# Kernel tuning notes

Hardware: AMD Instinct MI355X
Metric: run time of the kernel (lower is better)

## Reference

```python
import jax, jax.numpy as jnp
import numpy as np

B = 64        # num_groups
G = 32        # group_size
D = 2000      # output dim (counts per bin/gene)
M = 16        # m_samples
E = 16        # noise_dim
DIN = 256
LAM = 1.0
TRUST = 0.25
SMOOTH = 1e-8
IPF_ITERS = 60
EPS = 1e-12


def _arch(x, noise, W, b):
    # simple linear architecture: concat(x, noise) @ W + b
    return jnp.concatenate([x, noise], axis=-1) @ W + b


def _loss(x, target, W, b, noise_loss):
    # replicate each row m times (unsqueeze(1).expand(...).reshape == repeat)
    x_rep = jnp.repeat(x, M, axis=0)                      # [n*M, DIN]
    pred = _arch(x_rep, noise_loss, W, b)                 # [n*M, D] (no act_fn in loss path)
    pred = pred.reshape(B, G, M, D).sum(axis=1)           # [B, M, D]
    term_conf = jnp.linalg.norm(pred - target[:, None, :], axis=2).mean(axis=1)  # [B]
    sq = jnp.sum(pred * pred, axis=2)                     # [B, M]
    inn = jnp.einsum('bmd,bnd->bmn', pred, pred)          # [B, M, M]
    sqd = jnp.clip(sq[:, :, None] + sq[:, None, :] - 2.0 * inn, 1e-6)
    d = jnp.sqrt(sqd)
    mask = 1.0 - jnp.eye(M, dtype=d.dtype)
    mean_pd = jnp.sum(d * mask, axis=(1, 2)) / (M * (M - 1))
    return jnp.mean(term_conf - (LAM / 2.0) * mean_pd)


def _ipf(x_pred, C):
    # KL/I-projection with row anchoring (keep_rows=True, trust_clip=0.25)
    y = jnp.clip(x_pred, 0.0)
    C = jnp.clip(C.astype(y.dtype), 0.0)
    R = y.sum(axis=2)                                     # [B, G] anchor row totals
    col_zero = (y.sum(axis=1) <= 0) & (C > 0)
    y = y + SMOOTH * col_zero[:, None, :].astype(y.dtype)
    row_zero = (y.sum(axis=2) <= 0) & (R > 0)
    y = y + SMOOTH * row_zero[:, :, None].astype(y.dtype)

    def body(_, y):
        col = jnp.clip(y.sum(axis=1), EPS)
        y = y * jnp.clip(C / col, 1.0 - TRUST, 1.0 + TRUST)[:, None, :]
        row = jnp.clip(y.sum(axis=2), EPS)
        y = y * jnp.clip(R / row, 1.0 - TRUST, 1.0 + TRUST)[:, :, None]
        return y

    y = jax.lax.fori_loop(0, IPF_ITERS, body, y)
    col = jnp.clip(y.sum(axis=1), EPS)
    return y * (C / col)[:, None, :]


def _rank(v, descending):
    # rank along last axis via double argsort (0 = first picked)
    order = jnp.argsort(-v if descending else v, axis=-1)
    return jnp.argsort(order, axis=-1)


def _round_to_targets(x, target_bd):
    # exact integerization across G per (B, D); jit-safe full-G rank replaces dynamic-k topk+scatter
    x = jnp.clip(x, 0.0)
    xf = jnp.floor(x)
    y = xf.astype(jnp.int32)                              # [B, G, D]
    frac = x - xf
    need = target_bd - y.sum(axis=1)                      # [B, D]
    pos = jnp.clip(need, 0)
    q = pos // G
    y = y + q[:, None, :]
    r = pos - q * G
    rank = _rank(jnp.transpose(frac, (0, 2, 1)), descending=True)   # [B, D, G]
    add = (rank < r[:, :, None]).astype(jnp.int32)
    y = y + jnp.transpose(add, (0, 2, 1))
    # negative residuals: remove from smallest frac among y > 0
    need = target_bd - y.sum(axis=1)
    neg = jnp.clip(-need, 0)
    neg = jnp.minimum(neg, y.sum(axis=1))
    q = neg // G
    y_before = y
    y = jnp.clip(y - q[:, None, :], 0)
    removed = (y_before - y).sum(axis=1)
    r = neg - removed
    frac_m = jnp.where(y > 0, frac, jnp.inf)
    rank = _rank(jnp.transpose(frac_m, (0, 2, 1)), descending=False)
    rem = (rank < r[:, :, None]).astype(jnp.int32)
    y = jnp.clip(y - jnp.transpose(rem, (0, 2, 1)), 0)
    return y


def setup_inputs() -> dict:
    key = jax.random.key(0)
    ks = jax.random.split(key, 6)
    x = jax.random.normal(ks[0], (B * G, DIN), dtype=jnp.float32)
    target = jax.random.uniform(ks[1], (B, D), dtype=jnp.float32) * 100.0
    target_sum = jax.random.randint(ks[2], (B, D), 0, 200, dtype=jnp.int32)
    W = jax.random.normal(ks[3], (DIN + E, D), dtype=jnp.float32) * 0.02
    b = jnp.zeros((D,), dtype=jnp.float32)
    noise_loss = jax.random.normal(ks[4], (B * G * M, E), dtype=jnp.float32)
    noise_sample = jax.random.normal(ks[5], (B * G, E), dtype=jnp.float32)
    return {"x": x, "target": target, "target_sum": target_sum, "W": W, "b": b,
            "noise_loss": noise_loss, "noise_sample": noise_sample}


def reference(x, target, target_sum, W, b, noise_loss, noise_sample):
    loss = _loss(x, target, W, b, noise_loss)
    # conditional_sample pipeline (no-grad in original): softplus act (min_value==0)
    x_pred = jax.nn.softplus(_arch(x, noise_sample, W, b)).reshape(B, G, D)
    y_float = _ipf(x_pred, target_sum.astype(jnp.float32))
    y_int = _round_to_targets(y_float, target_sum.astype(jnp.int32))
    return loss, y_int.reshape(B * G, D)
```

## Files before the change

### kernel.cpp

```cpp
#include <hip/hip_runtime.h>
#include <math.h>

#define NB   64
#define NG   32
#define ND   2000
#define NM   16
#define NE   16
#define NDIN 256
#define NK   272

#define XPT_COLS 1152
#define SP_TAU   424
#define SP_F4_PER_B 6784
#define SMEM_MEGA (4096 + XPT_COLS * 128)

__device__ __forceinline__ float clampf(float v, float lo, float hi) {
    return fminf(fmaxf(v, lo), hi);
}

__device__ __forceinline__ float softplusf(float v) {
    return (v > 20.f) ? v : log1pf(expf(v));
}

__device__ __forceinline__ float readlane_f(float v, int lane) {
    return __int_as_float(__builtin_amdgcn_readlane(__float_as_int(v), lane));
}

__device__ __forceinline__ int sp_idx(int tau, int j, int k) {
    return (j * 8 + k) * SP_TAU + tau;
}

__device__ __forceinline__ int yget(const int* yvp, int g) {
    return (yvp[g >> 2] >> (8 * (g & 3))) & 0xff;
}
__device__ __forceinline__ void yadd(int* yvp, int g, int delta) {
    yvp[g >> 2] += delta << (8 * (g & 3));
}

__device__ __forceinline__ float wave_sum32(float v[NG], int lane) {
    {   const bool hi = (lane & 32) != 0;
        #pragma unroll
        for (int k = 0; k < 16; ++k) {
            float s = hi ? v[k] : v[k + 16];
            float r = __shfl_xor(s, 32);
            v[k] = (hi ? v[k + 16] : v[k]) + r;
        }
    }
    {   const bool hi = (lane & 16) != 0;
        #pragma unroll
        for (int k = 0; k < 8; ++k) {
            float s = hi ? v[k] : v[k + 8];
            float r = __shfl_xor(s, 16);
            v[k] = (hi ? v[k + 8] : v[k]) + r;
        }
    }
    {   const bool hi = (lane & 8) != 0;
        #pragma unroll
        for (int k = 0; k < 4; ++k) {
            float s = hi ? v[k] : v[k + 4];
            float r = __shfl_xor(s, 8);
            v[k] = (hi ? v[k + 4] : v[k]) + r;
        }
    }
    {   const bool hi = (lane & 4) != 0;
        #pragma unroll
        for (int k = 0; k < 2; ++k) {
            float s = hi ? v[k] : v[k + 2];
            float r = __shfl_xor(s, 4);
            v[k] = (hi ? v[k + 2] : v[k]) + r;
        }
    }
    {   const bool hi = (lane & 2) != 0;
        float s = hi ? v[0] : v[1];
        float r = __shfl_xor(s, 2);
        v[0] = (hi ? v[1] : v[0]) + r;
    }
    v[0] += __shfl_xor(v[0], 1);
    return v[0];
}

__device__ __forceinline__ void ipf_path(
        const float* __restrict__ xpT, const float* __restrict__ spB,
        const int* __restrict__ tsum, float* __restrict__ out,
        char* smem, int b, int t) {
    const int lane = t & 63, w = t >> 6;
    const bool lcls  = (t < 576);
    const bool valid = (t < 1000);
    const int g_own = (lane >> 1) & 31;
    const int rot = t & 7;
    const int tau = t - 576;
    const int c0 = lcls ? (2 * t) : (XPT_COLS + 2 * tau);

    float* wred = (float*)smem;
    char* cb = smem + 4096 + (size_t)c0 * 128;
    const float4* gx = (const float4*)(xpT + ((size_t)b * XPT_COLS + c0) * NG);
    const float4* gs = (const float4*)spB + (size_t)b * SP_F4_PER_B;

    float Cc0 = 0.f, Cc1 = 0.f;
    if (valid) {
        const int2 ci = *(const int2*)(tsum + (size_t)b * ND + c0);
        Cc0 = (float)ci.x; Cc1 = (float)ci.y;
    }
    float Ac0 = 1.f, Ac1 = 1.f;
    float Bown = 1.f, Rown;

    {
        float v[NG];
        if (lcls) {
            #pragma unroll
            for (int k = 0; k < 8; ++k) {
                const float4 a = gx[k], c = gx[8 + k];
                const int ro = 16 * ((k + rot) & 7);
                *(float4*)(cb + ro)       = a;
                *(float4*)(cb + 128 + ro) = c;
                v[4*k+0] = a.x + c.x;
                v[4*k+1] = a.y + c.y;
                v[4*k+2] = a.z + c.z;
                v[4*k+3] = a.w + c.w;
            }
        } else if (valid) {
            #pragma unroll
            for (int k = 0; k < 8; ++k) {
                const float4 a = gs[sp_idx(tau, 0, k)];
                const float4 c = gs[sp_idx(tau, 1, k)];
                v[4*k+0] = a.x + c.x;
                v[4*k+1] = a.y + c.y;
                v[4*k+2] = a.z + c.z;
                v[4*k+3] = a.w + c.w;
            }
        } else {
            #pragma unroll
            for (int g = 0; g < NG; ++g) v[g] = 0.f;
        }
        const float tot = wave_sum32(v, lane);
        if (!(lane & 1)) wred[w * NG + g_own] = tot;
        __syncthreads();
        float s = 0.f;
        #pragma unroll
        for (int w2 = 0; w2 < 16; ++w2) s += wred[w2 * NG + g_own];
        Rown = s;
    }

    for (int q = 1; q <= 60; ++q) {
        float s0 = 0.f, s1 = 0.f;
        if (lcls) {
            #pragma unroll
            for (int k = 0; k < 8; ++k) {
                const int ro = 16 * ((k + rot) & 7);
                const float4 a = *(const float4*)(cb + ro);
                const float4 c = *(const float4*)(cb + 128 + ro);
                float bg;
                bg = readlane_f(Bown, 8*k+0); s0 += a.x*bg; s1 += c.x*bg;
                bg = readlane_f(Bown, 8*k+2); s0 += a.y*bg; s1 += c.y*bg;
                bg = readlane_f(Bown, 8*k+4); s0 += a.z*bg; s1 += c.z*bg;
                bg = readlane_f(Bown, 8*k+6); s0 += a.w*bg; s1 += c.w*bg;
            }
        } else if (valid) {
            #pragma unroll
            for (int k = 0; k < 8; ++k) {
                const float4 a = gs[sp_idx(tau, 0, k)];
                const float4 c = gs[sp_idx(tau, 1, k)];
                float bg;
                bg = readlane_f(Bown, 8*k+0); s0 += a.x*bg; s1 += c.x*bg;
                bg = readlane_f(Bown, 8*k+2); s0 += a.y*bg; s1 += c.y*bg;
                bg = readlane_f(Bown, 8*k+4); s0 += a.z*bg; s1 += c.z*bg;
                bg = readlane_f(Bown, 8*k+6); s0 += a.w*bg; s1 += c.w*bg;
            }
        }
        Ac0 *= clampf(Cc0 / fmaxf(Ac0 * s0, 1e-12f), 0.75f, 1.25f);
        Ac1 *= clampf(Cc1 / fmaxf(Ac1 * s1, 1e-12f), 0.75f, 1.25f);

        asm volatile("" ::: "memory");

        float v[NG];
        if (lcls) {
            #pragma unroll
            for (int k = 0; k < 8; ++k) {
                const int ro = 16 * ((k + rot) & 7);
                const float4 a = *(const float4*)(cb + ro);
                const float4 c = *(const float4*)(cb + 128 + ro);
                v[4*k+0] = a.x * Ac0 + c.x * Ac1;
                v[4*k+1] = a.y * Ac0 + c.y * Ac1;
                v[4*k+2] = a.z * Ac0 + c.z * Ac1;
                v[4*k+3] = a.w * Ac0 + c.w * Ac1;
            }
        } else if (valid) {
            #pragma unroll
            for (int k = 0; k < 8; ++k) {
                const float4 a = gs[sp_idx(tau, 0, k)];
                const float4 c = gs[sp_idx(tau, 1, k)];
                v[4*k+0] = a.x * Ac0 + c.x * Ac1;
                v[4*k+1] = a.y * Ac0 + c.y * Ac1;
                v[4*k+2] = a.z * Ac0 + c.z * Ac1;
                v[4*k+3] = a.w * Ac0 + c.w * Ac1;
            }
        } else {
            #pragma unroll
            for (int g = 0; g < NG; ++g) v[g] = 0.f;
        }
        const float tot = wave_sum32(v, lane);
        const int buf = (q & 1) * (16 * NG);
        if (!(lane & 1)) wred[buf + w * NG + g_own] = tot;
        __syncthreads();
        float s = 0.f;
        #pragma unroll
        for (int w2 = 0; w2 < 16; ++w2) s += wred[buf + w2 * NG + g_own];
        Bown *= clampf(Rown / fmaxf(Bown * s, 1e-12f), 0.75f, 1.25f);
    }

    if (!valid) return;

    #pragma unroll
    for (int jj = 0; jj < 2; ++jj) {
        const int c = c0 + jj;
        const float A = jj ? Ac1 : Ac0;
        const int Ci = (int)(jj ? Cc1 : Cc0);
        const float Cf = (float)Ci;

        float c32[NG];
        if (lcls) {
            const char* basej = cb + jj * 128;
            #pragma unroll
            for (int k = 0; k < 8; ++k) {
                const float4 v4 = *(const float4*)(basej + 16 * ((k + rot) & 7));
                c32[4*k+0] = v4.x; c32[4*k+1] = v4.y;
                c32[4*k+2] = v4.z; c32[4*k+3] = v4.w;
            }
        } else {
            #pragma unroll
            for (int k = 0; k < 8; ++k) {
                const float4 v4 = gs[sp_idx(tau, jj, k)];
                c32[4*k+0] = v4.x; c32[4*k+1] = v4.y;
                c32[4*k+2] = v4.z; c32[4*k+3] = v4.w;
            }
        }

        float s = 0.f;
        #pragma unroll
        for (int g = 0; g < NG; ++g) {
            const float z = c32[g] * A * readlane_f(Bown, 2 * g);
            s += z;
            c32[g] = z;
        }
        const float F = Cf / fmaxf(s, 1e-12f);

        int yvp[8];
        #pragma unroll
        for (int i = 0; i < 8; ++i) yvp[i] = 0;
        int isum = 0;
        #pragma unroll
        for (int g = 0; g < NG; ++g) {
            const float y = c32[g] * F;
            const float fl = floorf(y);
            const int yi = (int)fl;
            c32[g] = y - fl;
            yadd(yvp, g, yi);
            isum += yi;
        }
        const int need = Ci - isum;
        const int pos = max(need, 0);
        const int qv = pos >> 5;
        const int rr = pos & 31;
        if (qv > 0) {
            #pragma unroll
            for (int i = 0; i < 8; ++i) yvp[i] += qv * 0x01010101;
        }
        #pragma unroll
        for (int g = 0; g < NG; ++g) {
            const float fg = c32[g];
            int rank = 0;
            #pragma unroll
            for (int h = 0; h < NG; ++h) {
                if (h == g) continue;
                const float fh = c32[h];
                rank += (h < g) ? (fh >= fg ? 1 : 0) : (fh > fg ? 1 : 0);
            }
            if (rank < rr) yadd(yvp, g, 1);
        }
        int neg = max(-need, 0);
        neg = min(neg, isum);
        if (__builtin_expect(neg > 0, 0)) {
            const int q2 = neg >> 5;
            int removed = 0;
            #pragma unroll
            for (int g = 0; g < NG; ++g) {
                const int yb = yget(yvp, g);
                const int yn = max(yb - q2, 0);
                removed += yb - yn;
                yadd(yvp, g, yn - yb);
            }
            const int r2 = neg - removed;
            if (r2 > 0) {
                const float INF = __builtin_inff();
                #pragma unroll
                for (int g = 0; g < NG; ++g) {
                    const float fg = (yget(yvp, g) > 0) ? c32[g] : INF;
                    int rank = 0;
                    #pragma unroll
                    for (int h = 0; h < NG; ++h) {
                        if (h == g) continue;
                        const float fh = (yget(yvp, h) > 0) ? c32[h] : INF;
                        rank += (h < g) ? (fh <= fg ? 1 : 0) : (fh < fg ? 1 : 0);
                    }
                    if (rank < r2) {
                        const int yb = yget(yvp, g);
                        yadd(yvp, g, max(yb - 1, 0) - yb);
                    }
                }
            }
        }
        #pragma unroll
        for (int g = 0; g < NG; ++g)
            out[1 + (size_t)(b * NG + g) * ND + c] = (float)yget(yvp, g);
    }
}

__device__ __forceinline__ void loss_path(
        const float* __restrict__ x, const float* __restrict__ nl,
        const float* __restrict__ tgt, const float* __restrict__ W,
        const float* __restrict__ bias, float* __restrict__ res2,
        float* smem, int cx, int b, int tt) {
    const int half = cx & 1;
    float* xsl = smem;
    float* nsl = smem + 256;
    float* tgl = smem + 512 + half * 4284;
    float* pt  = tgl + 252;

    if (half == 0 && tt < 256) {
        const float* xb = x + (size_t)b * NG * NDIN;
        float s = 0.f;
        for (int g = 0; g < NG; ++g) s += xb[g * NDIN + tt];
        xsl[tt] = s;
        const float* nb = nl + (size_t)b * NG * (NM * NE);
        float s2 = 0.f;
        for (int g = 0; g < NG; ++g) s2 += nb[g * (NM * NE) + tt];
        nsl[tt] = s2;
    }

    int tm = 0, tn = 0;
    if (tt >= 16 && tt < 152) {
        int p = tt - 16;
        for (int m = 0; m < NM; ++m) {
            int c = NM - m;
            if (p < c) { tm = m; tn = m + p; break; }
            p -= c;
        }
    }
    __syncthreads();

    const int d = cx * 250 + tt;
    if (tt < 250) {
        tgl[tt] = tgt[b * ND + d];
        float xw = 0.f;
        #pragma unroll 8
        for (int k = 0; k < NDIN; ++k) xw += xsl[k] * W[(size_t)k * ND + d];
        float we[NE];
        #pragma unroll
        for (int e = 0; e < NE; ++e) we[e] = W[(size_t)(NDIN + e) * ND + d];
        const float base0 = xw + (float)NG * bias[d];
        #pragma unroll
        for (int m = 0; m < NM; ++m) {
            float pm = base0;
            #pragma unroll
            for (int e = 0; e < NE; ++e) pm += nsl[m * NE + e] * we[e];
            pt[m * 252 + tt] = pm;
        }
    }
    if (tt < 32) {
        pt[(tt >> 1) * 252 + 250 + (tt & 1)] = 0.f;
        if (tt < 2) tgl[250 + tt] = 0.f;
    }
    __syncthreads();

    float acc = 0.f;
    if (tt < 16) {
        const float4* pa  = (const float4*)&pt[tt * 252];
        const float4* tga = (const float4*)&tgl[0];
        for (int i = 0; i < 63; ++i) {
            float4 pv = pa[i], tv = tga[i];
            float e0 = pv.x - tv.x, e1 = pv.y - tv.y, e2 = pv.z - tv.z, e3 = pv.w - tv.w;
            acc += e0 * e0 + e1 * e1 + e2 * e2 + e3 * e3;
        }
    } else if (tt < 152) {
        const float4* pa = (const float4*)&pt[tm * 252];
        const float4* pb = (const float4*)&pt[tn * 252];
        for (int i = 0; i < 63; ++i) {
            float4 u = pa[i], v = pb[i];
            acc += u.x * v.x + u.y * v.y + u.z * v.z + u.w * v.w;
        }
    }
    if (tt < 152) res2[((size_t)b * 8 + cx) * 152 + tt] = acc;
}

extern "C" __global__ __launch_bounds__(1024)
void mega(const float* __restrict__ x, const float* __restrict__ nl,
          const float* __restrict__ tgt, const float* __restrict__ W,
          const float* __restrict__ bias, const float* __restrict__ xpT,
          const float* __restrict__ spB, const int* __restrict__ tsum,
          float* __restrict__ out, float* __restrict__ res2) {
    extern __shared__ char smem[];
    const int bid = blockIdx.x;
    const int t = threadIdx.x;
    if (bid < NB) {
        ipf_path(xpT, spB, tsum, out, smem, bid, t);
    } else {
        const int l = bid - NB;
        #pragma unroll
        for (int rep = 0; rep < 2; ++rep) {
            const int slot = l + rep * 192;
            if (slot < 256) {
                __syncthreads();
                const int cx = ((slot & 3) << 1) | (t >> 9);
                loss_path(x, nl, tgt, W, bias, res2, (float*)smem,
                          cx, slot >> 2, t & 511);
            }
        }
    }
}

extern "C" __global__ __launch_bounds__(64)
void k2b_combine(const float* __restrict__ res2, float* __restrict__ out) {
    const int b = blockIdx.x, t = threadIdx.x;
    __shared__ float res[152];
    for (int tau = t; tau < 152; tau += 64) {
        float s = 0.f;
        #pragma unroll
        for (int c = 0; c < 8; ++c) s += res2[((size_t)b * 8 + c) * 152 + tau];
        res[tau] = s;
    }
    __syncthreads();
    if (t == 0) {
        float conf = 0.f;
        for (int m = 0; m < NM; ++m) conf += sqrtf(res[m]);
        conf *= (1.f / NM);
        float pd = 0.f;
        for (int m = 0; m < NM; ++m) {
            const int offm = 16 + m * NM - m * (m - 1) / 2;
            const float sqm = res[offm];
            for (int n = m + 1; n < NM; ++n) {
                const int offn = 16 + n * NM - n * (n - 1) / 2;
                const float sqn = res[offn];
                const float inn = res[offm + (n - m)];
                pd += sqrtf(fmaxf(sqm + sqn - 2.f * inn, 1e-6f));
            }
        }
        pd = 2.f * pd / (float)(NM * (NM - 1));
        atomicAdd(out, (conf - 0.5f * pd) * (1.f / NB));
    }
}

extern "C" __global__ __launch_bounds__(256)
void k3_xpred(const float* __restrict__ x, const float* __restrict__ nsamp,
              const float* __restrict__ W, const float* __restrict__ bias,
              float* __restrict__ xpT, float* __restrict__ spB,
              float* __restrict__ out) {
    const int dx = blockIdx.x;
    const int rb = blockIdx.y;
    const int t  = threadIdx.x;
    if (dx == 0 && rb == 0 && t == 0) out[0] = 0.f;
    __shared__ float xr[8][NK];
    #pragma unroll
    for (int r = 0; r < 8; ++r) {
        const int row = rb * 8 + r;
        xr[r][t] = x[(size_t)row * NDIN + t];
        if (t < NE) xr[r][NDIN + t] = nsamp[row * NE + t];
    }
    __syncthreads();
    if (t >= 250) return;
    const int d = dx * 1000 + 4 * t;
    float acc[8][4];
    #pragma unroll
    for (int r = 0; r < 8; ++r) {
        acc[r][0] = 0.f; acc[r][1] = 0.f; acc[r][2] = 0.f; acc[r][3] = 0.f;
    }
    for (int k = 0; k < NK; k += 4) {
        float4 w[4];
        #pragma unroll
        for (int kk = 0; kk < 4; ++kk) w[kk] = *(const float4*)&W[(size_t)(k + kk) * ND + d];
        #pragma unroll
        for (int r = 0; r < 8; ++r) {
            const float4 xv = *(const float4*)&xr[r][k];
            acc[r][0] += xv.x * w[0].x + xv.y * w[1].x + xv.z * w[2].x + xv.w * w[3].x;
            acc[r][1] += xv.x * w[0].y + xv.y * w[1].y + xv.z * w[2].y + xv.w * w[3].y;
            acc[r][2] += xv.x * w[0].z + xv.y * w[1].z + xv.z * w[2].z + xv.w * w[3].z;
            acc[r][3] += xv.x * w[0].w + xv.y * w[1].w + xv.z * w[2].w + xv.w * w[3].w;
        }
    }
    const float4 bv = *(const float4*)&bias[d];
    const float bvv[4] = {bv.x, bv.y, bv.z, bv.w};
    const int b2 = rb >> 2;
    const int g0 = (rb & 3) * 8;
    #pragma unroll
    for (int dd = 0; dd < 4; ++dd) {
        const int dc = d + dd;
        float4 lo, hi;
        lo.x = softplusf(acc[0][dd] + bvv[dd]);
        lo.y = softplusf(acc[1][dd] + bvv[dd]);
        lo.z = softplusf(acc[2][dd] + bvv[dd]);
        lo.w = softplusf(acc[3][dd] + bvv[dd]);
        hi.x = softplusf(acc[4][dd] + bvv[dd]);
        hi.y = softplusf(acc[5][dd] + bvv[dd]);
        hi.z = softplusf(acc[6][dd] + bvv[dd]);
        hi.w = softplusf(acc[7][dd] + bvv[dd]);
        if (dc < XPT_COLS) {
            float* op = xpT + ((size_t)b2 * XPT_COLS + dc) * NG + g0;
            *(float4*)op       = lo;
            *(float4*)(op + 4) = hi;
        } else {
            float4* sp = (float4*)spB + (size_t)b2 * SP_F4_PER_B;
            const int cc = dc - XPT_COLS;
            const int tau2 = cc >> 1, j = cc & 1;
            const int kk = g0 >> 2;
            sp[sp_idx(tau2, j, kk)]     = lo;
            sp[sp_idx(tau2, j, kk + 1)] = hi;
        }
    }
}

extern "C" void kernel_launch(void* const* d_in, const int* in_sizes, int n_in,
                              void* d_out, int out_size, void* d_ws, size_t ws_size,
                              hipStream_t stream) {
    const float* x     = (const float*)d_in[0];
    const float* tgt   = (const float*)d_in[1];
    const int*   tsum  = (const int*)d_in[2];
    const float* W     = (const float*)d_in[3];
    const float* bias  = (const float*)d_in[4];
    const float* nl    = (const float*)d_in[5];
    const float* nsamp = (const float*)d_in[6];
    float* out = (float*)d_out;

    (void)in_sizes; (void)n_in; (void)out_size; (void)ws_size;

    float* xpT  = (float*)d_ws;
    float* spB  = (float*)((char*)d_ws + 9437184);
    float* res2 = (float*)((char*)d_ws + 16384000);

    static int s_attr_done = 0;
    if (!s_attr_done) {
        hipFuncSetAttribute(reinterpret_cast<const void*>(mega),
                            hipFuncAttributeMaxDynamicSharedMemorySize,
                            SMEM_MEGA);
        s_attr_done = 1;
    }

    hipLaunchKernelGGL(k3_xpred, dim3(2, 256), dim3(256), 0, stream,
                       x, nsamp, W, bias, xpT, spB, out);
    hipLaunchKernelGGL(mega, dim3(256), dim3(1024), SMEM_MEGA, stream,
                       x, nl, tgt, W, bias, xpT, spB, tsum, out, res2);
    hipLaunchKernelGGL(k2b_combine, dim3(NB), dim3(64), 0, stream, res2, out);
}
```

Before: 364.2 us.

## Split IPF rounding epilogue out of mega kernel into separate wide-grid kernel

The per-column rounding epilogue (scale, floor, rank-based remainder distribution) moves out of the 64 IPF blocks of the mega kernel into a new k_epi kernel with an 8x64 grid of 256 threads. The mega kernel now only writes its per-column scale A and per-row scale B into the output buffer as scratch, and k_epi reads them back together with the cached xpT/spB predictions. This spreads the expensive 32x32 rank computation across far more blocks instead of serialising it in the tail of the 64 IPF blocks. The cost is an extra launch, re-reading the predictions from global memory, and relying on the output buffer as a temporary that k_epi later overwrites.

Result: faster. 344.6 us (-5.4%).

```diff
diff --git a/kernel.cpp b/kernel.cpp
--- a/kernel.cpp
+++ b/kernel.cpp
@@ -208,110 +208,14 @@
         Bown *= clampf(Rown / fmaxf(Bown * s, 1e-12f), 0.75f, 1.25f);
     }
 
-    if (!valid) return;
-
-    #pragma unroll
-    for (int jj = 0; jj < 2; ++jj) {
-        const int c = c0 + jj;
-        const float A = jj ? Ac1 : Ac0;
-        const int Ci = (int)(jj ? Cc1 : Cc0);
-        const float Cf = (float)Ci;
-
-        float c32[NG];
-        if (lcls) {
-            const char* basej = cb + jj * 128;
-            #pragma unroll
-            for (int k = 0; k < 8; ++k) {
-                const float4 v4 = *(const float4*)(basej + 16 * ((k + rot) & 7));
-                c32[4*k+0] = v4.x; c32[4*k+1] = v4.y;
-                c32[4*k+2] = v4.z; c32[4*k+3] = v4.w;
-            }
-        } else {
-            #pragma unroll
-            for (int k = 0; k < 8; ++k) {
-                const float4 v4 = gs[sp_idx(tau, jj, k)];
-                c32[4*k+0] = v4.x; c32[4*k+1] = v4.y;
-                c32[4*k+2] = v4.z; c32[4*k+3] = v4.w;
-            }
-        }
-
-        float s = 0.f;
-        #pragma unroll
-        for (int g = 0; g < NG; ++g) {
-            const float z = c32[g] * A * readlane_f(Bown, 2 * g);
-            s += z;
-            c32[g] = z;
-        }
-        const float F = Cf / fmaxf(s, 1e-12f);
-
-        int yvp[8];
-        #pragma unroll
-        for (int i = 0; i < 8; ++i) yvp[i] = 0;
-        int isum = 0;
-        #pragma unroll
-        for (int g = 0; g < NG; ++g) {
-            const float y = c32[g] * F;
-            const float fl = floorf(y);
-            const int yi = (int)fl;
-            c32[g] = y - fl;
-            yadd(yvp, g, yi);
-            isum += yi;
-        }
-        const int need = Ci - isum;
-        const int pos = max(need, 0);
-        const int qv = pos >> 5;
-        const int rr = pos & 31;
-        if (qv > 0) {
-            #pragma unroll
-            for (int i = 0; i < 8; ++i) yvp[i] += qv * 0x01010101;
-        }
-        #pragma unroll
-        for (int g = 0; g < NG; ++g) {
-            const float fg = c32[g];
-            int rank = 0;
-            #pragma unroll
-            for (int h = 0; h < NG; ++h) {
-                if (h == g) continue;
-                const float fh = c32[h];
-                rank += (h < g) ? (fh >= fg ? 1 : 0) : (fh > fg ? 1 : 0);
-            }
-            if (rank < rr) yadd(yvp, g, 1);
-        }
-        int neg = max(-need, 0);
-        neg = min(neg, isum);
-        if (__builtin_expect(neg > 0, 0)) {
-            const int q2 = neg >> 5;
-            int removed = 0;
-            #pragma unroll
-            for (int g = 0; g < NG; ++g) {
-                const int yb = yget(yvp, g);
-                const int yn = max(yb - q2, 0);
-                removed += yb - yn;
-                yadd(yvp, g, yn - yb);
-            }
-            const int r2 = neg - removed;
-            if (r2 > 0) {
-                const float INF = __builtin_inff();
-                #pragma unroll
-                for (int g = 0; g < NG; ++g) {
-                    const float fg = (yget(yvp, g) > 0) ? c32[g] : INF;
-                    int rank = 0;
-                    #pragma unroll
-                    for (int h = 0; h < NG; ++h) {
-                        if (h == g) continue;
-                        const float fh = (yget(yvp, h) > 0) ? c32[h] : INF;
-                        rank += (h < g) ? (fh <= fg ? 1 : 0) : (fh < fg ? 1 : 0);
-                    }
-                    if (rank < r2) {
-                        const int yb = yget(yvp, g);
-                        yadd(yvp, g, max(yb - 1, 0) - yb);
-                    }
-                }
-            }
-        }
-        #pragma unroll
-        for (int g = 0; g < NG; ++g)
-            out[1 + (size_t)(b * NG + g) * ND + c] = (float)yget(yvp, g);
+    if (valid) {
+        float* ap = out + 1 + (size_t)(b * NG) * ND + c0;
+        ap[0] = Ac0; ap[1] = Ac1;
+    }
+    if (w == 0 && !(lane & 1)) {
+        #pragma unroll
+        for (int qq = 0; qq < 8; ++qq)
+            out[1 + (size_t)(b * NG + 1) * ND + qq * 250 + g_own] = Bown;
     }
 }
 
@@ -416,6 +320,124 @@
             }
         }
     }
+}
+
+extern "C" __global__ __launch_bounds__(256)
+void k_epi(const float* __restrict__ xpT, const float* __restrict__ spB,
+           const int* __restrict__ tsum, float* __restrict__ out) {
+    const int chunk = blockIdx.x;
+    const int b     = blockIdx.y;
+    const int tt    = threadIdx.x;
+    __shared__ float bf[NG];
+
+    if (tt < NG)
+        bf[tt] = out[1 + (size_t)(b * NG + 1) * ND + chunk * 250 + tt];
+    __syncthreads();
+    if (tt >= 250) return;
+
+    const int c = chunk * 250 + tt;
+    const float A = out[1 + (size_t)(b * NG) * ND + c];
+    const int Ci = tsum[(size_t)b * ND + c];
+    const float Cf = (float)Ci;
+
+    float c32[NG];
+    if (c < XPT_COLS) {
+        const float4* cp = (const float4*)(xpT + ((size_t)b * XPT_COLS + c) * NG);
+        #pragma unroll
+        for (int k = 0; k < 8; ++k) {
+            const float4 v = cp[k];
+            c32[4*k+0] = v.x; c32[4*k+1] = v.y;
+            c32[4*k+2] = v.z; c32[4*k+3] = v.w;
+        }
+    } else {
+        const float4* gsp = (const float4*)spB + (size_t)b * SP_F4_PER_B;
+        const int cc = c - XPT_COLS;
+        const int tau2 = cc >> 1, j = cc & 1;
+        #pragma unroll
+        for (int k = 0; k < 8; ++k) {
+            const float4 v = gsp[sp_idx(tau2, j, k)];
+            c32[4*k+0] = v.x; c32[4*k+1] = v.y;
+            c32[4*k+2] = v.z; c32[4*k+3] = v.w;
+        }
+    }
+
+    float s = 0.f;
+    #pragma unroll
+    for (int g = 0; g < NG; ++g) {
+        const float z = c32[g] * A * bf[g];
+        s += z;
+        c32[g] = z;
+    }
+    const float F = Cf / fmaxf(s, 1e-12f);
+
+    int yvp[8];
+    #pragma unroll
+    for (int i = 0; i < 8; ++i) yvp[i] = 0;
+    int isum = 0;
+    #pragma unroll
+    for (int g = 0; g < NG; ++g) {
+        const float y = c32[g] * F;
+        const float fl = floorf(y);
+        const int yi = (int)fl;
+        c32[g] = y - fl;
+        yadd(yvp, g, yi);
+        isum += yi;
+    }
+    const int need = Ci - isum;
+    const int pos = max(need, 0);
+    const int qv = pos >> 5;
+    const int rr = pos & 31;
+    if (qv > 0) {
+        #pragma unroll
+        for (int i = 0; i < 8; ++i) yvp[i] += qv * 0x01010101;
+    }
+    #pragma unroll
+    for (int g = 0; g < NG; ++g) {
+        const float fg = c32[g];
+        int rank = 0;
+        #pragma unroll
+        for (int h = 0; h < NG; ++h) {
+            if (h == g) continue;
+            const float fh = c32[h];
+            rank += (h < g) ? (fh >= fg ? 1 : 0) : (fh > fg ? 1 : 0);
+        }
+        if (rank < rr) yadd(yvp, g, 1);
+    }
+    int neg = max(-need, 0);
+    neg = min(neg, isum);
+    if (__builtin_expect(neg > 0, 0)) {
+        const int q2 = neg >> 5;
+        int removed = 0;
+        #pragma unroll
+        for (int g = 0; g < NG; ++g) {
+            const int yb = yget(yvp, g);
+            const int yn = max(yb - q2, 0);
+            removed += yb - yn;
+            yadd(yvp, g, yn - yb);
+        }
+        const int r2 = neg - removed;
+        if (r2 > 0) {
+            const float INF = __builtin_inff();
+            #pragma unroll
+            for (int g = 0; g < NG; ++g) {
+                const float fg = (yget(yvp, g) > 0) ? c32[g] : INF;
+                int rank = 0;
+                #pragma unroll
+                for (int h = 0; h < NG; ++h) {
+                    if (h == g) continue;
+                    const float fh = (yget(yvp, h) > 0) ? c32[h] : INF;
+                    rank += (h < g) ? (fh <= fg ? 1 : 0) : (fh < fg ? 1 : 0);
+                }
+                if (rank < r2) {
+                    const int yb = yget(yvp, g);
+                    yadd(yvp, g, max(yb - 1, 0) - yb);
+                }
+            }
+        }
+    }
+    #pragma unroll
+    for (int g = 0; g < NG; ++g)
+        out[1 + (size_t)(b * NG + g) * ND + c] = (float)yget(yvp, g);
 }
 
 extern "C" __global__ __launch_bounds__(64)
@@ -547,5 +569,7 @@
                        x, nsamp, W, bias, xpT, spB, out);
     hipLaunchKernelGGL(mega, dim3(256), dim3(1024), SMEM_MEGA, stream,
                        x, nl, tgt, W, bias, xpT, spB, tsum, out, res2);
+    hipLaunchKernelGGL(k_epi, dim3(8, 64), dim3(256), 0, stream,
+                       xpT, spB, tsum, out);
     hipLaunchKernelGGL(k2b_combine, dim3(NB), dim3(64), 0, stream, res2, out);
 }
```
